# Kernel tuning notes

Hardware: AMD Instinct MI355X
Metric: run time of the kernel (lower is better)

Reference implementation:

```python
import jax, jax.numpy as jnp
import numpy as np

D_MODEL = 1024
D_FF = 4096
N_EXPERTS = 8
TOP_K = 2

def setup_inputs() -> dict:
    key = jax.random.key(0)
    ks = jax.random.split(key, 8)
    s = 0.02
    return {
        "x": jax.random.normal(ks[0], (4, 2048, D_MODEL), dtype=jnp.float32),
        "W1": jax.random.normal(ks[1], (N_EXPERTS, D_MODEL, D_FF), dtype=jnp.float32) * s,
        "b1": jnp.zeros((N_EXPERTS, D_FF), dtype=jnp.float32),
        "W2": jax.random.normal(ks[2], (N_EXPERTS, D_FF, D_MODEL), dtype=jnp.float32) * s,
        "b2": jnp.zeros((N_EXPERTS, D_MODEL), dtype=jnp.float32),
        "Wg": jax.random.normal(ks[3], (D_MODEL, N_EXPERTS), dtype=jnp.float32) * s,
        "bg": jnp.zeros((N_EXPERTS,), dtype=jnp.float32),
    }

def reference(x, W1, b1, W2, b2, Wg, bg):
    B, S, D = x.shape
    # Gating network
    gate_logits = jnp.einsum('bsd,de->bse', x, Wg) + bg
    gate_probs = jax.nn.softmax(gate_logits, axis=-1)  # (B,S,E)
    # Top-k routing on softmax probs (matches torch.topk(F.softmax(logits)))
    top_k_probs, top_k_indices = jax.lax.top_k(gate_probs, TOP_K)  # (B,S,k)
    T = B * S
    x_flat = x.reshape(T, D)
    idx_flat = top_k_indices.reshape(T, TOP_K)
    prob_flat = top_k_probs.reshape(T, TOP_K)
    # Per-token combine weight for each expert: sum of top-k probs routed to it
    # combine[t, e] = sum_j prob_flat[t, j] * (idx_flat[t, j] == e)
    onehot = jax.nn.one_hot(idx_flat, N_EXPERTS, dtype=x.dtype)  # (T,k,E)
    combine = jnp.einsum('tk,tke->te', prob_flat, onehot)  # (T,E)
    out = jnp.zeros((T, D), dtype=x.dtype)
    for e in range(N_EXPERTS):  # static small loop over experts
        h = jax.nn.relu(x_flat @ W1[e] + b1[e])  # (T, d_ff)
        y = h @ W2[e] + b2[e]                    # (T, d_model)
        out = out + combine[:, e:e+1] * y
    return out.reshape(B, S, D), gate_probs
```

## Files before the change

kernel.cpp:

```cpp
#include <hip/hip_runtime.h>

#define D_MODEL 1024
#define D_FF    4096
#define N_EXP   8
#define BM 128
#define BN 256
#define BK 32

typedef __attribute__((ext_vector_type(8))) short bf16x8;
typedef __attribute__((ext_vector_type(4))) float f32x4;
typedef unsigned int u32;

__device__ __forceinline__ unsigned short f2bf(float f) {
  union { float f; unsigned u; } v; v.f = f;
  unsigned r = v.u + 0x7FFFu + ((v.u >> 16) & 1u);
  return (unsigned short)(r >> 16);
}

__device__ __forceinline__ void gl_lds16(const void* g, void* l) {
  __builtin_amdgcn_global_load_lds((const __attribute__((address_space(1))) u32*)g,
                                   (__attribute__((address_space(3))) u32*)l, 16, 0, 0);
}

__global__ __launch_bounds__(256)
void transpose_convert_all(const float* __restrict__ W1, const float* __restrict__ W2,
                           unsigned short* __restrict__ w1t, unsigned short* __restrict__ w2t) {
  __shared__ u32 s32k[128][65];
  int b = blockIdx.x;
  const float* se;
  unsigned short* de;
  int Ksub, Nsrc;
  if (b < 2048) {
    int kt = b & 3, nt = (b >> 2) & 63, e = b >> 8;
    Ksub = D_MODEL; Nsrc = D_FF;
    se = W1 + (size_t)e * D_MODEL * D_FF + (size_t)(kt * 256) * D_FF + nt * 64;
    de = w1t + (size_t)e * D_FF * D_MODEL + (size_t)(nt * 64) * D_MODEL + kt * 256;
  } else {
    int b2 = b - 2048;
    int kt = b2 & 15, nt = (b2 >> 4) & 15, e = b2 >> 8;
    Ksub = D_FF; Nsrc = D_MODEL;
    se = W2 + (size_t)e * D_FF * D_MODEL + (size_t)(kt * 256) * D_MODEL + nt * 64;
    de = w2t + (size_t)e * D_MODEL * D_FF + (size_t)(nt * 64) * D_FF + kt * 256;
  }
  int tid = threadIdx.x;
  int kh = tid >> 4;
  int n4 = (tid & 15) * 4;
  #pragma unroll
  for (int p = 0; p < 8; p++) {
    int k = kh * 2 + p * 32;
    float4 v0 = *(const float4*)(se + (size_t)k * Nsrc + n4);
    float4 v1 = *(const float4*)(se + (size_t)(k + 1) * Nsrc + n4);
    #pragma unroll
    for (int j = 0; j < 4; j++) {
      u32 pk = (u32)f2bf(((const float*)&v0)[j]) |
               ((u32)f2bf(((const float*)&v1)[j]) << 16);
      s32k[kh + p * 16][n4 + j] = pk;
    }
  }
  __syncthreads();
  #pragma unroll
  for (int c = 0; c < 8; c++) {
    int id = tid + c * 256;
    int n = id >> 5;
    int kc = id & 31;
    uint4 o;
    o.x = s32k[kc * 4 + 0][n];
    o.y = s32k[kc * 4 + 1][n];
    o.z = s32k[kc * 4 + 2][n];
    o.w = s32k[kc * 4 + 3][n];
    *(uint4*)(de + (size_t)n * Ksub + kc * 8) = o;
  }
}

__global__ void gating_kernel(const float* __restrict__ x,
                              const float* __restrict__ Wg,
                              const float* __restrict__ bg,
                              float* __restrict__ gate_out,
                              unsigned short* __restrict__ xb,
                              int* __restrict__ cnt,
                              int* __restrict__ tokIdx,
                              float* __restrict__ tokW, int T) {
  int wv = threadIdx.x >> 6, lane = threadIdx.x & 63;
  int t = blockIdx.x * 4 + wv;
  if (t >= T) return;
  const float* xr = x + (size_t)t * D_MODEL + lane * 16;
  float acc[N_EXP];
  #pragma unroll
  for (int e = 0; e < N_EXP; e++) acc[e] = 0.f;
  ushort4 xc[4];
  #pragma unroll
  for (int q = 0; q < 4; q++) {
    float4 xv = *(const float4*)(xr + q * 4);
    xc[q].x = f2bf(xv.x); xc[q].y = f2bf(xv.y);
    xc[q].z = f2bf(xv.z); xc[q].w = f2bf(xv.w);
    #pragma unroll
    for (int r = 0; r < 4; r++) {
      float xs = ((const float*)&xv)[r];
      const float* wrow = Wg + (size_t)(lane * 16 + q * 4 + r) * N_EXP;
      float4 wa = *(const float4*)wrow;
      float4 wb = *(const float4*)(wrow + 4);
      acc[0] += xs * wa.x; acc[1] += xs * wa.y; acc[2] += xs * wa.z; acc[3] += xs * wa.w;
      acc[4] += xs * wb.x; acc[5] += xs * wb.y; acc[6] += xs * wb.z; acc[7] += xs * wb.w;
    }
  }
  unsigned short* xbr = xb + (size_t)t * D_MODEL + lane * 16;
  #pragma unroll
  for (int q = 0; q < 4; q++) *(ushort4*)(xbr + q * 4) = xc[q];
  #pragma unroll
  for (int off = 32; off > 0; off >>= 1) {
    #pragma unroll
    for (int e = 0; e < N_EXP; e++) acc[e] += __shfl_xor(acc[e], off);
  }
  if (lane == 0) {
    float l[N_EXP], p[N_EXP];
    float m = -1e30f;
    #pragma unroll
    for (int e = 0; e < N_EXP; e++) { l[e] = acc[e] + bg[e]; m = fmaxf(m, l[e]); }
    float s = 0.f;
    #pragma unroll
    for (int e = 0; e < N_EXP; e++) { p[e] = __expf(l[e] - m); s += p[e]; }
    float inv = 1.f / s;
    #pragma unroll
    for (int e = 0; e < N_EXP; e++) { p[e] *= inv; gate_out[(size_t)t * N_EXP + e] = p[e]; }
    int e1 = 0;
    #pragma unroll
    for (int e = 1; e < N_EXP; e++) if (p[e] > p[e1]) e1 = e;
    int e2 = (e1 == 0) ? 1 : 0;
    #pragma unroll
    for (int e = 0; e < N_EXP; e++) if (e != e1 && p[e] > p[e2]) e2 = e;
    int pos = atomicAdd(cnt + e1, 1);
    tokIdx[(size_t)e1 * T + pos] = t; tokW[(size_t)e1 * T + pos] = p[e1];
    pos = atomicAdd(cnt + e2, 1);
    tokIdx[(size_t)e2 * T + pos] = t; tokW[(size_t)e2 * T + pos] = p[e2];
  }
}

__global__ void schedule_kernel(const int* __restrict__ cnt, int* __restrict__ meta,
                                int* __restrict__ tE, int* __restrict__ tB,
                                int* __restrict__ tV, int T, int maxTiles) {
  if (threadIdx.x != 0 || blockIdx.x != 0) return;
  int t = 0;
  for (int e = 0; e < N_EXP; e++) {
    int c = cnt[e];
    for (int r = 0; r < c && t < maxTiles; r += BM) {
      tE[t] = e; tB[t] = e * T + r; tV[t] = min(BM, c - r); t++;
    }
  }
  meta[0] = t;
}

#define STAGE(b, kt) { \
    gl_lds16(srcA0 + (size_t)(kt) * BK, &LDSU[(b) * 12288 + w * 512]); \
    gl_lds16(srcB0 + (size_t)(kt) * BK, &LDSU[(b) * 12288 + 4096 + w * 1024]); \
    gl_lds16(srcB1 + (size_t)(kt) * BK, &LDSU[(b) * 12288 + 4096 + w * 1024 + 512]); }

#define COMPUTE(b) { \
    bf16x8 ra[4], rbv[4]; \
    _Pragma("unroll") for (int m_ = 0; m_ < 4; m_++) { \
      int row_ = wr * 64 + m_ * 16 + l15; \
      ra[m_] = *(const bf16x8*)&LDSU[(b) * 12288 + row_ * 32 + (((l4 + (row_ >> 1)) & 3) << 3)]; } \
    _Pragma("unroll") for (int n_ = 0; n_ < 4; n_++) { \
      int rb_ = wc * 64 + n_ * 16 + l15; \
      rbv[n_] = *(const bf16x8*)&LDSU[(b) * 12288 + 4096 + rb_ * 32 + (((l4 + (rb_ >> 1)) & 3) << 3)]; } \
    _Pragma("unroll") for (int m_ = 0; m_ < 4; m_++) \
      _Pragma("unroll") for (int n_ = 0; n_ < 4; n_++) \
        acc[m_][n_] = __builtin_amdgcn_mfma_f32_16x16x32_bf16(ra[m_], rbv[n_], acc[m_][n_], 0, 0, 0); }

#define BAR() { __builtin_amdgcn_s_barrier(); asm volatile("" ::: "memory"); }
#define WAITVM(N) asm volatile("s_waitcnt vmcnt(" #N ")" ::: "memory");

#define PIPE3(NT) \
  STAGE(0, 0); STAGE(1, 1); \
  for (int it = 0; it < ((NT) - 2) / 3; it++) { \
    int kt = 3 * it; \
    STAGE(2, kt + 2); WAITVM(6); BAR(); COMPUTE(0); BAR(); \
    STAGE(0, kt + 3); WAITVM(6); BAR(); COMPUTE(1); BAR(); \
    STAGE(1, kt + 4); WAITVM(6); BAR(); COMPUTE(2); BAR(); \
  } \
  WAITVM(3); BAR(); COMPUTE(0); BAR(); \
  WAITVM(0); BAR(); COMPUTE(1);

#define ACC_INIT() f32x4 acc[4][4]; \
  _Pragma("unroll") for (int m = 0; m < 4; m++) \
    _Pragma("unroll") for (int n = 0; n < 4; n++) acc[m][n] = (f32x4){0.f, 0.f, 0.f, 0.f};

__global__ __launch_bounds__(512)
void gemm1_kernel(const unsigned short* __restrict__ xb,
                  const unsigned short* __restrict__ w1t,
                  const float* __restrict__ b1,
                  const int* __restrict__ meta,
                  const int* __restrict__ tE, const int* __restrict__ tB,
                  const int* __restrict__ tV, const int* __restrict__ tokIdx,
                  unsigned short* __restrict__ h, int nT) {
  __shared__ unsigned short LDSU[36864];

  int total = gridDim.x;
  int L = blockIdx.x;
  int q = total >> 3, r8 = total & 7;
  int xcd = L & 7, idx = L >> 3;
  int work = (xcd < r8) ? (xcd * (q + 1) + idx) : (r8 * (q + 1) + (xcd - r8) * q + idx);
  int cb = work / nT;
  int tile = work - cb * nT;
  if (tile >= meta[0]) return;
  int e = tE[tile], base = tB[tile], valid = tV[tile];
  int tid = threadIdx.x;

  int w = tid >> 6, lane = tid & 63;
  int wr = w >> 2, wc = w & 3;
  int l15 = lane & 15, l4 = lane >> 4;
  int sr = lane >> 2, lch = lane & 3;

  const unsigned short* panel = w1t + (size_t)e * D_FF * D_MODEL;
  int rA = w * 16 + sr;
  int tokS = tokIdx[base + (rA < valid ? rA : valid - 1)];
  int gA = (lch - (rA >> 1)) & 3;
  const unsigned short* srcA0 = xb + (size_t)tokS * D_MODEL + gA * 8;
  int rB0 = w * 32 + sr;
  int gB0 = (lch - (rB0 >> 1)) & 3;
  const unsigned short* srcB0 = panel + (size_t)(cb * BN + rB0) * D_MODEL + gB0 * 8;
  int rB1 = w * 32 + 16 + sr;
  int gB1 = (lch - (rB1 >> 1)) & 3;
  const unsigned short* srcB1 = panel + (size_t)(cb * BN + rB1) * D_MODEL + gB1 * 8;

  ACC_INIT();
  PIPE3(D_MODEL / BK);

  #pragma unroll
  for (int n = 0; n < 4; n++) {
    int colc = cb * BN + wc * 64 + n * 16 + l15;
    float bias = b1[(size_t)e * D_FF + colc];
    #pragma unroll
    for (int m = 0; m < 4; m++) {
      #pragma unroll
      for (int r = 0; r < 4; r++) {
        int row = wr * 64 + m * 16 + l4 * 4 + r;
        float v = acc[m][n][r] + bias;
        v = v > 0.f ? v : 0.f;
        h[(size_t)(tile * BM + row) * D_FF + colc] = f2bf(v);
      }
    }
  }
}

__global__ __launch_bounds__(512)
void gemm2_kernel(const unsigned short* __restrict__ h,
                  const unsigned short* __restrict__ w2t,
                  const float* __restrict__ b2,
                  const int* __restrict__ meta,
                  const int* __restrict__ tE, const int* __restrict__ tB,
                  const int* __restrict__ tV, const int* __restrict__ tokIdx,
                  const float* __restrict__ tokW,
                  float* __restrict__ out) {
  __shared__ unsigned short LDSU[36864];

  int total = gridDim.x;
  int L = blockIdx.x;
  int q = total >> 3, r8 = total & 7;
  int xcd = L & 7, idx = L >> 3;
  int work = (xcd < r8) ? (xcd * (q + 1) + idx) : (r8 * (q + 1) + (xcd - r8) * q + idx);
  int tile = work >> 2;
  int cb = work & 3;
  if (tile >= meta[0]) return;
  int e = tE[tile], base = tB[tile], valid = tV[tile];
  int tid = threadIdx.x;

  int w = tid >> 6, lane = tid & 63;
  int wr = w >> 2, wc = w & 3;
  int l15 = lane & 15, l4 = lane >> 4;
  int sr = lane >> 2, lch = lane & 3;

  const unsigned short* panel = w2t + (size_t)e * D_MODEL * D_FF;
  int rA = w * 16 + sr;
  int gA = (lch - (rA >> 1)) & 3;
  const unsigned short* srcA0 = h + (size_t)(tile * BM + rA) * D_FF + gA * 8;
  int rB0 = w * 32 + sr;
  int gB0 = (lch - (rB0 >> 1)) & 3;
  const unsigned short* srcB0 = panel + (size_t)(cb * BN + rB0) * D_FF + gB0 * 8;
  int rB1 = w * 32 + 16 + sr;
  int gB1 = (lch - (rB1 >> 1)) & 3;
  const unsigned short* srcB1 = panel + (size_t)(cb * BN + rB1) * D_FF + gB1 * 8;

  ACC_INIT();
  PIPE3(D_FF / BK);

  float biasv[4];
  #pragma unroll
  for (int n = 0; n < 4; n++)
    biasv[n] = b2[(size_t)e * D_MODEL + cb * BN + wc * 64 + n * 16 + l15];

  #pragma unroll
  for (int m = 0; m < 4; m++) {
    #pragma unroll
    for (int r = 0; r < 4; r++) {
      int row = wr * 64 + m * 16 + l4 * 4 + r;
      if (row < valid) {
        int tok = tokIdx[base + row];
        float wgt = tokW[base + row];
        float* orow = out + (size_t)tok * D_MODEL + cb * BN + wc * 64 + l15;
        #pragma unroll
        for (int n = 0; n < 4; n++)
          atomicAdd(orow + n * 16, (acc[m][n][r] + biasv[n]) * wgt);
      }
    }
  }
}

extern "C" void kernel_launch(void* const* d_in, const int* in_sizes, int n_in,
                              void* d_out, int out_size, void* d_ws, size_t ws_size,
                              hipStream_t stream) {
  const float* x  = (const float*)d_in[0];
  const float* W1 = (const float*)d_in[1];
  const float* b1 = (const float*)d_in[2];
  const float* W2 = (const float*)d_in[3];
  const float* b2 = (const float*)d_in[4];
  const float* Wg = (const float*)d_in[5];
  const float* bg = (const float*)d_in[6];

  int T = in_sizes[0] / D_MODEL;
  float* out = (float*)d_out;
  float* gate_out = out + (size_t)T * D_MODEL;

  char* ws = (char*)d_ws;
  int* cnt  = (int*)(ws + 0);
  int* meta = (int*)(ws + 64);
  int* tE   = (int*)(ws + 128);
  int* tB   = (int*)(ws + 1024);
  int* tV   = (int*)(ws + 2048);
  size_t off = 4096;
  int* tokIdx = (int*)(ws + off);   off += (size_t)N_EXP * T * 4;
  float* tokW = (float*)(ws + off); off += (size_t)N_EXP * T * 4;
  unsigned short* xb = (unsigned short*)(ws + off); off += (size_t)T * D_MODEL * 2;
  off = (off + 255) & ~(size_t)255;

  int maxTiles = (2 * T) / BM + N_EXP;

  unsigned short* w1t = (unsigned short*)(ws + off); off += (size_t)N_EXP * D_MODEL * D_FF * 2;
  unsigned short* w2t = (unsigned short*)(ws + off); off += (size_t)N_EXP * D_MODEL * D_FF * 2;
  unsigned short* h   = (unsigned short*)(ws + off);

  hipMemsetAsync(d_out, 0, (size_t)T * D_MODEL * sizeof(float), stream);
  hipMemsetAsync(cnt, 0, N_EXP * sizeof(int), stream);

  gating_kernel<<<(T + 3) / 4, 256, 0, stream>>>(x, Wg, bg, gate_out, xb, cnt, tokIdx, tokW, T);
  schedule_kernel<<<1, 64, 0, stream>>>(cnt, meta, tE, tB, tV, T, maxTiles);

  transpose_convert_all<<<4096, 256, 0, stream>>>(W1, W2, w1t, w2t);

  gemm1_kernel<<<maxTiles * (D_FF / BN), 512, 0, stream>>>(
      xb, w1t, b1, meta, tE, tB, tV, tokIdx, h, maxTiles);
  gemm2_kernel<<<maxTiles * (D_MODEL / BN), 512, 0, stream>>>(
      h, w2t, b2, meta, tE, tB, tV, tokIdx, tokW, out);
}
```

Measured before the change: 681.2 us.

## Convert both expert GEMMs into persistent kernels with per-XCD strided work loops

```diff
diff --git a/kernel.cpp b/kernel.cpp
--- a/kernel.cpp
+++ b/kernel.cpp
@@ -194,51 +194,53 @@
                   unsigned short* __restrict__ h, int nT) {
   __shared__ unsigned short LDSU[36864];
 
-  int total = gridDim.x;
-  int L = blockIdx.x;
-  int q = total >> 3, r8 = total & 7;
-  int xcd = L & 7, idx = L >> 3;
-  int work = (xcd < r8) ? (xcd * (q + 1) + idx) : (r8 * (q + 1) + (xcd - r8) * q + idx);
-  int cb = work / nT;
-  int tile = work - cb * nT;
-  if (tile >= meta[0]) return;
-  int e = tE[tile], base = tB[tile], valid = tV[tile];
+  const int WPX = (136 * (D_FF / BN)) / 8;
+  int xcd = blockIdx.x & 7, idx = blockIdx.x >> 3;
   int tid = threadIdx.x;
-
   int w = tid >> 6, lane = tid & 63;
   int wr = w >> 2, wc = w & 3;
   int l15 = lane & 15, l4 = lane >> 4;
   int sr = lane >> 2, lch = lane & 3;
-
-  const unsigned short* panel = w1t + (size_t)e * D_FF * D_MODEL;
-  int rA = w * 16 + sr;
-  int tokS = tokIdx[base + (rA < valid ? rA : valid - 1)];
-  int gA = (lch - (rA >> 1)) & 3;
-  const unsigned short* srcA0 = xb + (size_t)tokS * D_MODEL + gA * 8;
-  int rB0 = w * 32 + sr;
-  int gB0 = (lch - (rB0 >> 1)) & 3;
-  const unsigned short* srcB0 = panel + (size_t)(cb * BN + rB0) * D_MODEL + gB0 * 8;
-  int rB1 = w * 32 + 16 + sr;
-  int gB1 = (lch - (rB1 >> 1)) & 3;
-  const unsigned short* srcB1 = panel + (size_t)(cb * BN + rB1) * D_MODEL + gB1 * 8;
-
-  ACC_INIT();
-  PIPE3(D_MODEL / BK);
-
-  #pragma unroll
-  for (int n = 0; n < 4; n++) {
-    int colc = cb * BN + wc * 64 + n * 16 + l15;
-    float bias = b1[(size_t)e * D_FF + colc];
-    #pragma unroll
-    for (int m = 0; m < 4; m++) {
+  int nTiles = meta[0];
+
+  for (int wk = idx; wk < WPX; wk += 64) {
+    int work = xcd * WPX + wk;
+    int cb = work / nT;
+    int tile = work - cb * nT;
+    if (tile >= nTiles) continue;
+    int e = tE[tile], base = tB[tile], valid = tV[tile];
+
+    const unsigned short* panel = w1t + (size_t)e * D_FF * D_MODEL;
+    int rA = w * 16 + sr;
+    int tokS = tokIdx[base + (rA < valid ? rA : valid - 1)];
+    int gA = (lch - (rA >> 1)) & 3;
+    const unsigned short* srcA0 = xb + (size_t)tokS * D_MODEL + gA * 8;
+    int rB0 = w * 32 + sr;
+    int gB0 = (lch - (rB0 >> 1)) & 3;
+    const unsigned short* srcB0 = panel + (size_t)(cb * BN + rB0) * D_MODEL + gB0 * 8;
+    int rB1 = w * 32 + 16 + sr;
+    int gB1 = (lch - (rB1 >> 1)) & 3;
+    const unsigned short* srcB1 = panel + (size_t)(cb * BN + rB1) * D_MODEL + gB1 * 8;
+
+    ACC_INIT();
+    PIPE3(D_MODEL / BK);
+
+    #pragma unroll
+    for (int n = 0; n < 4; n++) {
+      int colc = cb * BN + wc * 64 + n * 16 + l15;
+      float bias = b1[(size_t)e * D_FF + colc];
       #pragma unroll
-      for (int r = 0; r < 4; r++) {
-        int row = wr * 64 + m * 16 + l4 * 4 + r;
-        float v = acc[m][n][r] + bias;
-        v = v > 0.f ? v : 0.f;
-        h[(size_t)(tile * BM + row) * D_FF + colc] = f2bf(v);
+      for (int m = 0; m < 4; m++) {
+        #pragma unroll
+        for (int r = 0; r < 4; r++) {
+          int row = wr * 64 + m * 16 + l4 * 4 + r;
+          float v = acc[m][n][r] + bias;
+          v = v > 0.f ? v : 0.f;
+          h[(size_t)(tile * BM + row) * D_FF + colc] = f2bf(v);
+        }
       }
     }
+    BAR();
   }
 }
 
@@ -253,55 +255,57 @@
                   float* __restrict__ out) {
   __shared__ unsigned short LDSU[36864];
 
-  int total = gridDim.x;
-  int L = blockIdx.x;
-  int q = total >> 3, r8 = total & 7;
-  int xcd = L & 7, idx = L >> 3;
-  int work = (xcd < r8) ? (xcd * (q + 1) + idx) : (r8 * (q + 1) + (xcd - r8) * q + idx);
-  int tile = work >> 2;
-  int cb = work & 3;
-  if (tile >= meta[0]) return;
-  int e = tE[tile], base = tB[tile], valid = tV[tile];
+  const int WPX = (136 * (D_MODEL / BN)) / 8;
+  int xcd = blockIdx.x & 7, idx = blockIdx.x >> 3;
   int tid = threadIdx.x;
-
   int w = tid >> 6, lane = tid & 63;
   int wr = w >> 2, wc = w & 3;
   int l15 = lane & 15, l4 = lane >> 4;
   int sr = lane >> 2, lch = lane & 3;
-
-  const unsigned short* panel = w2t + (size_t)e * D_MODEL * D_FF;
-  int rA = w * 16 + sr;
-  int gA = (lch - (rA >> 1)) & 3;
-  const unsigned short* srcA0 = h + (size_t)(tile * BM + rA) * D_FF + gA * 8;
-  int rB0 = w * 32 + sr;
-  int gB0 = (lch - (rB0 >> 1)) & 3;
-  const unsigned short* srcB0 = panel + (size_t)(cb * BN + rB0) * D_FF + gB0 * 8;
-  int rB1 = w * 32 + 16 + sr;
-  int gB1 = (lch - (rB1 >> 1)) & 3;
-  const unsigned short* srcB1 = panel + (size_t)(cb * BN + rB1) * D_FF + gB1 * 8;
-
-  ACC_INIT();
-  PIPE3(D_FF / BK);
-
-  float biasv[4];
-  #pragma unroll
-  for (int n = 0; n < 4; n++)
-    biasv[n] = b2[(size_t)e * D_MODEL + cb * BN + wc * 64 + n * 16 + l15];
-
-  #pragma unroll
-  for (int m = 0; m < 4; m++) {
-    #pragma unroll
-    for (int r = 0; r < 4; r++) {
-      int row = wr * 64 + m * 16 + l4 * 4 + r;
-      if (row < valid) {
-        int tok = tokIdx[base + row];
-        float wgt = tokW[base + row];
-        float* orow = out + (size_t)tok * D_MODEL + cb * BN + wc * 64 + l15;
-        #pragma unroll
-        for (int n = 0; n < 4; n++)
-          atomicAdd(orow + n * 16, (acc[m][n][r] + biasv[n]) * wgt);
+  int nTiles = meta[0];
+
+  for (int wk = idx; wk < WPX; wk += 64) {
+    int work = xcd * WPX + wk;
+    int tile = work >> 2;
+    int cb = work & 3;
+    if (tile >= nTiles) continue;
+    int e = tE[tile], base = tB[tile], valid = tV[tile];
+
+    const unsigned short* panel = w2t + (size_t)e * D_MODEL * D_FF;
+    int rA = w * 16 + sr;
+    int gA = (lch - (rA >> 1)) & 3;
+    const unsigned short* srcA0 = h + (size_t)(tile * BM + rA) * D_FF + gA * 8;
+    int rB0 = w * 32 + sr;
+    int gB0 = (lch - (rB0 >> 1)) & 3;
+    const unsigned short* srcB0 = panel + (size_t)(cb * BN + rB0) * D_FF + gB0 * 8;
+    int rB1 = w * 32 + 16 + sr;
+    int gB1 = (lch - (rB1 >> 1)) & 3;
+    const unsigned short* srcB1 = panel + (size_t)(cb * BN + rB1) * D_FF + gB1 * 8;
+
+    ACC_INIT();
+    PIPE3(D_FF / BK);
+
+    float biasv[4];
+    #pragma unroll
+    for (int n = 0; n < 4; n++)
+      biasv[n] = b2[(size_t)e * D_MODEL + cb * BN + wc * 64 + n * 16 + l15];
+
+    #pragma unroll
+    for (int m = 0; m < 4; m++) {
+      #pragma unroll
+      for (int r = 0; r < 4; r++) {
+        int row = wr * 64 + m * 16 + l4 * 4 + r;
+        if (row < valid) {
+          int tok = tokIdx[base + row];
+          float wgt = tokW[base + row];
+          float* orow = out + (size_t)tok * D_MODEL + cb * BN + wc * 64 + l15;
+          #pragma unroll
+          for (int n = 0; n < 4; n++)
+            atomicAdd(orow + n * 16, (acc[m][n][r] + biasv[n]) * wgt);
+        }
       }
     }
+    BAR();
   }
 }
 
@@ -346,8 +350,8 @@
 
   transpose_convert_all<<<4096, 256, 0, stream>>>(W1, W2, w1t, w2t);
 
-  gemm1_kernel<<<maxTiles * (D_FF / BN), 512, 0, stream>>>(
+  gemm1_kernel<<<512, 512, 0, stream>>>(
       xb, w1t, b1, meta, tE, tB, tV, tokIdx, h, maxTiles);
-  gemm2_kernel<<<maxTiles * (D_MODEL / BN), 512, 0, stream>>>(
+  gemm2_kernel<<<512, 512, 0, stream>>>(
       h, w2t, b2, meta, tE, tB, tV, tokIdx, tokW, out);
 }
```

After: 730.8 us. 7.3% more time.
